# Performance work log

Hardware: AMD Instinct MI355X
Metric: run time of the kernel (lower is better)

Reference implementation:

```python
import jax, jax.numpy as jnp
import numpy as np


def _shift(w):
    # max(0, -min(w)): scalar shift making w + shift non-negative
    return jnp.maximum(0.0, -jnp.min(w))


def shifted_linear(x, W, b=None):
    # F.linear with non-negative weights plus row-sum correction
    alpha = _shift(W)
    y = x @ (W + alpha).T - alpha * jnp.sum(x, axis=-1, keepdims=True)
    if b is not None:
        y = y + b
    return y


def shifted_depthwise_conv(x, w, b):
    # x: (B, D, L), w: (D, 1, K) depthwise; causal-style padding K-1, sliced to L by caller
    alpha = _shift(w)
    k = w.shape[2]
    pad = k - 1
    dn = ('NCH', 'OIH', 'NCH')
    groups = w.shape[0]
    y = jax.lax.conv_general_dilated(x, w + alpha, (1,), [(pad, pad)],
                                     dimension_numbers=dn, feature_group_count=groups)
    ones_k = jnp.ones_like(w)
    ssum = jax.lax.conv_general_dilated(x, ones_k, (1,), [(pad, pad)],
                                        dimension_numbers=dn, feature_group_count=groups)
    return y - alpha * ssum + b[None, :, None]


def setup_inputs() -> dict:
    key = jax.random.key(0)
    ks = jax.random.split(key, 10)
    d_model, d_inner, d_state, d_conv, dt_rank = 1024, 2048, 16, 4, 64
    B, L = 2, 1024
    s = 0.05
    return {
        'hidden_states': jax.random.normal(ks[0], (B, L, d_model), jnp.float32),
        'W_in': jax.random.normal(ks[1], (2 * d_inner, d_model), jnp.float32) * s,
        'conv_w': jax.random.normal(ks[2], (d_inner, 1, d_conv), jnp.float32) * 0.3,
        'conv_b': jax.random.normal(ks[3], (d_inner,), jnp.float32) * s,
        'W_x': jax.random.normal(ks[4], (dt_rank + 2 * d_state, d_inner), jnp.float32) * s,
        'W_dt': jax.random.normal(ks[5], (d_inner, dt_rank), jnp.float32) * s,
        'dt_bias': jax.random.normal(ks[6], (d_inner,), jnp.float32),
        'W_out': jax.random.normal(ks[7], (d_model, d_inner), jnp.float32) * s,
        'A_log': jax.random.normal(ks[8], (d_inner, d_state), jnp.float32) * 0.5,
        'D': jax.random.normal(ks[9], (d_inner,), jnp.float32),
    }


def reference(hidden_states, W_in, conv_w, conv_b, W_x, W_dt, dt_bias, W_out, A_log, D):
    b, l, dm = hidden_states.shape
    d_inner = conv_w.shape[0]
    d_state = A_log.shape[1]
    dt_rank = W_dt.shape[1]

    A = jnp.exp(A_log)  # (d_inner, d_state), always positive

    # in_proj over (b*l, d_model) -> (b, 2*d_inner, l)
    xz = shifted_linear(hidden_states.reshape(b * l, dm), W_in)
    xz = xz.reshape(b, l, 2 * d_inner).transpose(0, 2, 1)
    x, z = xz[:, :d_inner], xz[:, d_inner:]

    # depthwise shifted conv + SiLU activation, truncated to seqlen
    x = jax.nn.silu(shifted_depthwise_conv(x, conv_w, conv_b)[..., :l])

    # x_proj -> dt_raw, B, C
    x_dbl = shifted_linear(x.transpose(0, 2, 1).reshape(b * l, d_inner), W_x)
    dt_raw = x_dbl[:, :dt_rank]
    Bm = x_dbl[:, dt_rank:dt_rank + d_state].reshape(b, l, d_state).transpose(0, 2, 1)  # (b,n,l)
    Cm = x_dbl[:, dt_rank + d_state:].reshape(b, l, d_state).transpose(0, 2, 1)         # (b,n,l)
    dt = shifted_linear(dt_raw, W_dt).reshape(b, l, d_inner).transpose(0, 2, 1)          # (b,d,l)

    # delta activation (softplus) with bias, clamped
    delta = jnp.clip(jax.nn.softplus(dt + dt_bias[None, :, None]), 1e-4, 20.0)

    # global scalar shifts for B and C
    beta = _shift(Bm)
    gamma = _shift(Cm)
    B_nn = Bm + beta
    C_nn = Cm + gamma

    # precomputed per-step operands, scan axis first: (l, b, d, n)
    deltaA = jnp.exp(-jnp.einsum('bdl,dn->lbdn', delta, A))
    dBu = jnp.einsum('bdl,bnl,bdl->lbdn', delta, B_nn, x)
    C_scan = C_nn.transpose(2, 0, 1)  # (l, b, n)

    def step(xc, inp):
        dA_i, dBu_i, C_i = inp
        xc = dA_i * xc + dBu_i                                   # (b,d,n)
        y = jnp.einsum('bdn,bn->bd', xc, C_i) - gamma * jnp.sum(xc, axis=-1)
        return xc, y

    x0 = jnp.zeros((b, d_inner, d_state), dtype=delta.dtype)
    _, ys = jax.lax.scan(step, x0, (deltaA, dBu, C_scan))        # ys: (l, b, d)

    y = ys.transpose(1, 2, 0) + x * D[None, :, None]             # (b, d, l) skip term
    y = y * jax.nn.silu(z)                                       # gate activation

    out = shifted_linear(y.transpose(0, 2, 1).reshape(b * l, d_inner), W_out)
    return out.reshape(b, l, dm)
```

## Files before the change

kernel.cpp:

```cpp
#include <hip/hip_runtime.h>
#include <hip/hip_bf16.h>
#include <math.h>

#define DM 1024
#define DI 2048
#define DS 16
#define DTR 64
#define NB 2
#define LL 1024
#define TT (NB*LL)
#define SCH 16
#define NCH (LL/SCH)

typedef unsigned short u16;
typedef __attribute__((ext_vector_type(8))) short bf16x8;
typedef __attribute__((ext_vector_type(4))) float f32x4;

#define LOG2E 1.4426950408889634f

__device__ inline u16 f2bf(float f) {
  union { float f; unsigned u; } c; c.f = f;
  unsigned u = c.u;
  return (u16)((u + 0x7fffu + ((u >> 16) & 1u)) >> 16);
}

#define GLDS16(g, l) __builtin_amdgcn_global_load_lds( \
    (const __attribute__((address_space(1))) unsigned int*)(g), \
    (__attribute__((address_space(3))) unsigned int*)(l), 16, 0, 0)

template<int BM, int BN>
__global__ __launch_bounds__(256) void gemm_bf16(
    const u16* __restrict__ A, const u16* __restrict__ B,
    float* __restrict__ C, int M, int N, int K) {
  constexpr int WAVES_M = BM / 64;
  constexpr int WAVES_N = 4 / WAVES_M;
  constexpr int WTM = 4;
  constexpr int WTN = BN / (WAVES_N * 16);
  constexpr int ASLABS = BM / 16;
  constexpr int SLABS = (BM + BN) / 16;
  constexpr int SPW = SLABS / 4;
  __shared__ u16 As[BM * 32];
  __shared__ u16 Bs[BN * 32];
  const int tid = threadIdx.x;
  const int wave = tid >> 6;
  const int lane = tid & 63;
  const int bm = blockIdx.y * BM;
  const int bn = blockIdx.x * BN;
  const int wm = (wave / WAVES_N) * 64;
  const int wn = (wave % WAVES_N) * (WTN * 16);
  const int r4 = lane >> 2;
  const int kc = (lane & 3) * 8;
  const int fr = lane & 15;
  const int fq = lane >> 4;

  f32x4 acc[WTM][WTN];
#pragma unroll
  for (int i = 0; i < WTM; ++i)
#pragma unroll
    for (int j = 0; j < WTN; ++j) acc[i][j] = (f32x4){0.f, 0.f, 0.f, 0.f};

  for (int k0 = 0; k0 < K; k0 += 32) {
#pragma unroll
    for (int s = wave * SPW; s < (wave + 1) * SPW; ++s) {
      if (s < ASLABS) {
        int row = s * 16 + r4;
        GLDS16(A + (size_t)(bm + row) * K + k0 + kc, &As[s * 512]);
      } else {
        int row = (s - ASLABS) * 16 + r4;
        GLDS16(B + (size_t)(bn + row) * K + k0 + kc, &Bs[(s - ASLABS) * 512]);
      }
    }
    __syncthreads();
    bf16x8 af[WTM], bf[WTN];
#pragma unroll
    for (int i = 0; i < WTM; ++i)
      af[i] = *(const bf16x8*)&As[(wm + 16 * i + fr) * 32 + fq * 8];
#pragma unroll
    for (int j = 0; j < WTN; ++j)
      bf[j] = *(const bf16x8*)&Bs[(wn + 16 * j + fr) * 32 + fq * 8];
#pragma unroll
    for (int i = 0; i < WTM; ++i)
#pragma unroll
      for (int j = 0; j < WTN; ++j)
        acc[i][j] = __builtin_amdgcn_mfma_f32_16x16x32_bf16(af[i], bf[j], acc[i][j], 0, 0, 0);
    __syncthreads();
  }

#pragma unroll
  for (int i = 0; i < WTM; ++i) {
    int row0 = bm + wm + 16 * i + fq * 4;
#pragma unroll
    for (int j = 0; j < WTN; ++j) {
      int col = bn + wn + 16 * j + fr;
#pragma unroll
      for (int r = 0; r < 4; ++r)
        C[(size_t)(row0 + r) * N + col] = acc[i][j][r];
    }
  }
}

template<int EPI>
__global__ __launch_bounds__(256) void gemm_bt(
    const float* __restrict__ A, const float* __restrict__ B,
    float* __restrict__ C, int M, int N,
    int lda, int ldb, int ldc, const float* __restrict__ bias, int kz) {
  __shared__ float As[16][65];
  __shared__ float Bs[16][65];
  const int tid = threadIdx.x;
  const int bm = blockIdx.y * 64;
  const int bn = blockIdx.x * 64;
  const int ty = tid >> 4;
  const int tx = tid & 15;
  const int koff = blockIdx.z * kz;
  C += (size_t)blockIdx.z * M * ldc;
  float acc[4][4] = {{0.f}};

  for (int k0 = koff; k0 < koff + kz; k0 += 16) {
#pragma unroll
    for (int i = 0; i < 4; ++i) {
      int e = tid + 256 * i;
      int r = e >> 4, c = e & 15;
      As[c][r] = A[(size_t)(bm + r) * lda + k0 + c];
    }
#pragma unroll
    for (int i = 0; i < 4; ++i) {
      int e = tid + 256 * i;
      int r = e >> 4, c = e & 15;
      int gn = bn + r;
      Bs[c][r] = (gn < N) ? B[(size_t)gn * ldb + k0 + c] : 0.0f;
    }
    __syncthreads();
#pragma unroll
    for (int k = 0; k < 16; ++k) {
      float a[4], bb[4];
#pragma unroll
      for (int i = 0; i < 4; ++i) a[i] = As[k][ty + 16 * i];
#pragma unroll
      for (int j = 0; j < 4; ++j) bb[j] = Bs[k][tx + 16 * j];
#pragma unroll
      for (int i = 0; i < 4; ++i)
#pragma unroll
        for (int j = 0; j < 4; ++j) acc[i][j] += a[i] * bb[j];
    }
    __syncthreads();
  }

#pragma unroll
  for (int i = 0; i < 4; ++i) {
    int m = bm + ty + 16 * i;
#pragma unroll
    for (int j = 0; j < 4; ++j) {
      int n = bn + tx + 16 * j;
      if (n < N) {
        float v = acc[i][j];
        if (EPI == 1) {
          v += bias[n];
          float sp = (v > 20.0f) ? v : log1pf(expf(v));
          v = fminf(fmaxf(sp, 1e-4f), 20.0f);
        }
        C[(size_t)m * ldc + n] = v;
      }
    }
  }
}

__global__ __launch_bounds__(256) void gemm3_reduce(
    const float* __restrict__ part, float* __restrict__ xdb) {
  int i = blockIdx.x * 256 + threadIdx.x;
  float s = 0.f;
#pragma unroll
  for (int z = 0; z < 8; ++z) s += part[(size_t)z * TT * 96 + i];
  xdb[i] = s;
}

__global__ __launch_bounds__(256) void cast_all(
    const float* __restrict__ hs, const float* __restrict__ win,
    const float* __restrict__ wout, u16* __restrict__ hs_bf,
    u16* __restrict__ win_bf, u16* __restrict__ wout_bf) {
  int gid = blockIdx.x * 256 + threadIdx.x;
  const float* src; u16* dst; int off;
  if (gid < 524288)        { src = hs;   dst = hs_bf;   off = gid; }
  else if (gid < 1572864)  { src = win;  dst = win_bf;  off = gid - 524288; }
  else                     { src = wout; dst = wout_bf; off = gid - 1572864; }
  float4 v = ((const float4*)src)[off];
  ushort4 o;
  o.x = f2bf(v.x); o.y = f2bf(v.y); o.z = f2bf(v.z); o.w = f2bf(v.w);
  ((ushort4*)dst)[off] = o;
}

__global__ __launch_bounds__(256) void conv_silu4(
    const float* __restrict__ xz, const float* __restrict__ w,
    const float* __restrict__ cb, float* __restrict__ xc) {
  int gid = blockIdx.x * 256 + threadIdx.x;
  int dq = (gid & 511) * 4;
  int t = gid >> 9;
  int l = t & (LL - 1);
  float wv[4][4];
#pragma unroll
  for (int j = 0; j < 4; ++j) {
    float4 ww = *(const float4*)&w[(dq + j) * 4];
    wv[j][0] = ww.x; wv[j][1] = ww.y; wv[j][2] = ww.z; wv[j][3] = ww.w;
  }
  float4 acc = *(const float4*)&cb[dq];
#pragma unroll
  for (int k = 0; k < 4; ++k) {
    int ll = l - 3 + k;
    if (ll < 0) continue;
    float4 xv = *(const float4*)&xz[(size_t)(t - 3 + k) * (2 * DI) + dq];
    acc.x += xv.x * wv[0][k]; acc.y += xv.y * wv[1][k];
    acc.z += xv.z * wv[2][k]; acc.w += xv.w * wv[3][k];
  }
  acc.x /= (1.0f + expf(-acc.x)); acc.y /= (1.0f + expf(-acc.y));
  acc.z /= (1.0f + expf(-acc.z)); acc.w /= (1.0f + expf(-acc.w));
  *(float4*)&xc[(size_t)t * DI + dq] = acc;
}

__global__ __launch_bounds__(256) void beta_part(
    const float* __restrict__ xdb, float* __restrict__ pmin) {
  float mn = 3.4e38f;
  for (int i = blockIdx.x * 256 + threadIdx.x; i < TT * DS; i += 64 * 256) {
    int t = i >> 4, n = i & 15;
    mn = fminf(mn, xdb[t * 96 + 64 + n]);
  }
#pragma unroll
  for (int o = 32; o; o >>= 1) mn = fminf(mn, __shfl_down(mn, o));
  __shared__ float sm[4];
  if ((threadIdx.x & 63) == 0) sm[threadIdx.x >> 6] = mn;
  __syncthreads();
  if (threadIdx.x == 0)
    pmin[blockIdx.x] = fminf(fminf(sm[0], sm[1]), fminf(sm[2], sm[3]));
}

__global__ void beta_fin(const float* __restrict__ pmin, float* __restrict__ beta) {
  float mn = pmin[threadIdx.x];
#pragma unroll
  for (int o = 32; o; o >>= 1) mn = fminf(mn, __shfl_down(mn, o));
  if (threadIdx.x == 0) beta[0] = fmaxf(0.0f, -mn);
}

__global__ __launch_bounds__(256) void scan_pass1(
    const float* __restrict__ delta, const float* __restrict__ xc,
    const float* __restrict__ xdb, const float* __restrict__ A_log,
    const float* __restrict__ beta_p,
    float* __restrict__ hend, float* __restrict__ Ssum) {
  const int d = blockIdx.x * 256 + threadIdx.x;
  const int c = blockIdx.y;
  const int b = blockIdx.z;
  __shared__ float Bsh[SCH][16];
  const float beta = beta_p[0];
  const int t0 = b * LL + c * SCH;
  {
    int i = threadIdx.x;
    int tt = i >> 4, n = i & 15;
    Bsh[tt][n] = xdb[(size_t)(t0 + tt) * 96 + 64 + n] + beta;
  }
  __syncthreads();
  float Av2[16];
#pragma unroll
  for (int n = 0; n < 16; ++n) Av2[n] = expf(A_log[d * 16 + n]) * LOG2E;
  float h[16];
#pragma unroll
  for (int n = 0; n < 16; ++n) h[n] = 0.f;
  float S = 0.f;
  for (int tt = 0; tt < SCH; ++tt) {
    int t = t0 + tt;
    float dv = delta[(size_t)t * DI + d];
    float xv = xc[(size_t)t * DI + d];
    float dx = dv * xv;
    S += dv;
#pragma unroll
    for (int n = 0; n < 16; ++n) {
      float a = __builtin_amdgcn_exp2f(-dv * Av2[n]);
      h[n] = a * h[n] + dx * Bsh[tt][n];
    }
  }
  size_t base = (((size_t)(b * NCH + c) * DI) + d) * 16;
#pragma unroll
  for (int n = 0; n < 16; ++n) hend[base + n] = h[n];
  Ssum[((size_t)(b * NCH + c) * DI) + d] = S;
}

__global__ __launch_bounds__(256) void scan_pass2(
    float* __restrict__ hend, const float* __restrict__ Ssum,
    const float* __restrict__ A_log) {
  int gid = blockIdx.x * 256 + threadIdx.x;
  int n = gid & 15;
  int d = (gid >> 4) & (DI - 1);
  int b = gid >> 15;
  float Av2 = expf(A_log[d * 16 + n]) * LOG2E;
  float H = 0.f;
  for (int c = 0; c < NCH; ++c) {
    size_t cb = ((size_t)(b * NCH + c) * DI) + d;
    float hl = hend[cb * 16 + n];
    float p = __builtin_amdgcn_exp2f(-Av2 * Ssum[cb]);
    hend[cb * 16 + n] = H;
    H = p * H + hl;
  }
}

__global__ __launch_bounds__(256) void scan_pass3(
    const float* __restrict__ delta, const float* __restrict__ xc,
    const float* __restrict__ xdb, const float* __restrict__ xz,
    const float* __restrict__ A_log, const float* __restrict__ Dp,
    const float* __restrict__ beta_p, const float* __restrict__ hstart,
    u16* __restrict__ ybf) {
  const int d = blockIdx.x * 256 + threadIdx.x;
  const int c = blockIdx.y;
  const int b = blockIdx.z;
  __shared__ float Bsh[SCH][16];
  __shared__ float Csh[SCH][16];
  const float beta = beta_p[0];
  const int t0 = b * LL + c * SCH;
  {
    int i = threadIdx.x;
    int tt = i >> 4, n = i & 15;
    size_t row = (size_t)(t0 + tt) * 96;
    Bsh[tt][n] = xdb[row + 64 + n] + beta;
    Csh[tt][n] = xdb[row + 80 + n];
  }
  __syncthreads();
  float Av2[16];
#pragma unroll
  for (int n = 0; n < 16; ++n) Av2[n] = expf(A_log[d * 16 + n]) * LOG2E;
  float h[16];
  size_t base = (((size_t)(b * NCH + c) * DI) + d) * 16;
#pragma unroll
  for (int n = 0; n < 16; ++n) h[n] = hstart[base + n];
  const float Dd = Dp[d];
  for (int tt = 0; tt < SCH; ++tt) {
    int t = t0 + tt;
    float dv = delta[(size_t)t * DI + d];
    float xv = xc[(size_t)t * DI + d];
    float dx = dv * xv;
    float yv = 0.f;
#pragma unroll
    for (int n = 0; n < 16; ++n) {
      float a = __builtin_amdgcn_exp2f(-dv * Av2[n]);
      h[n] = a * h[n] + dx * Bsh[tt][n];
      yv += h[n] * Csh[tt][n];
    }
    float zv = xz[(size_t)t * (2 * DI) + DI + d];
    float out = (yv + xv * Dd) * (zv / (1.0f + expf(-zv)));
    ybf[(size_t)t * DI + d] = f2bf(out);
  }
}

extern "C" void kernel_launch(void* const* d_in, const int* in_sizes, int n_in,
                              void* d_out, int out_size, void* d_ws, size_t ws_size,
                              hipStream_t stream) {
  const float* hs      = (const float*)d_in[0];
  const float* W_in    = (const float*)d_in[1];
  const float* conv_w  = (const float*)d_in[2];
  const float* conv_b  = (const float*)d_in[3];
  const float* W_x     = (const float*)d_in[4];
  const float* W_dt    = (const float*)d_in[5];
  const float* dt_bias = (const float*)d_in[6];
  const float* W_out   = (const float*)d_in[7];
  const float* A_log   = (const float*)d_in[8];
  const float* Dp      = (const float*)d_in[9];
  float* out = (float*)d_out;

  float* ws     = (float*)d_ws;
  float* xz     = ws;
  float* xcv    = xz   + (size_t)TT * 2 * DI;
  float* xdb    = xcv  + (size_t)TT * DI;
  float* dlt    = xdb  + (size_t)TT * 96;
  float* betab  = dlt  + (size_t)TT * DI;
  float* pmin   = betab + 64;
  float* hend   = pmin + 64;
  float* Ssum   = hend + (size_t)NB * NCH * DI * 16;
  float* hs_bfR = Ssum + (size_t)NB * NCH * DI;
  float* win_bfR  = hs_bfR + (size_t)TT * DM / 2;
  float* wout_bfR = win_bfR + (size_t)2 * DI * DM / 2;

  u16* hs_bf   = (u16*)hs_bfR;
  u16* win_bf  = (u16*)win_bfR;
  u16* wout_bf = (u16*)wout_bfR;
  u16* ybf     = (u16*)win_bfR;
  float* part  = dlt;

  dim3 blk(256);

  cast_all<<<8192, blk, 0, stream>>>(hs, W_in, W_out, hs_bf, win_bf, wout_bf);

  gemm_bf16<128, 128><<<dim3(4096 / 128, TT / 128), blk, 0, stream>>>(
      hs_bf, win_bf, xz, TT, 2 * DI, DM);

  conv_silu4<<<(TT * DI / 4) / 256, blk, 0, stream>>>(xz, conv_w, conv_b, xcv);

  gemm_bt<0><<<dim3(2, TT / 64, 8), blk, 0, stream>>>(
      xcv, W_x, part, TT, 96, DI, DI, 96, nullptr, 256);
  gemm3_reduce<<<(TT * 96) / 256, blk, 0, stream>>>(part, xdb);

  beta_part<<<64, blk, 0, stream>>>(xdb, pmin);
  beta_fin<<<1, 64, 0, stream>>>(pmin, betab);

  gemm_bt<1><<<dim3(DI / 64, TT / 64), blk, 0, stream>>>(
      xdb, W_dt, dlt, TT, DI, 96, DTR, DI, dt_bias, DTR);

  scan_pass1<<<dim3(DI / 256, NCH, NB), blk, 0, stream>>>(
      dlt, xcv, xdb, A_log, betab, hend, Ssum);
  scan_pass2<<<(NB * DI * DS) / 256, blk, 0, stream>>>(hend, Ssum, A_log);
  scan_pass3<<<dim3(DI / 256, NCH, NB), blk, 0, stream>>>(
      dlt, xcv, xdb, xz, A_log, Dp, betab, hend, ybf);

  gemm_bf16<64, 128><<<dim3(DM / 128, TT / 64), blk, 0, stream>>>(
      ybf, wout_bf, out, TT, DM, DI);
}
```

Measured before the change: 293.3 us.

## Move x_proj and dt_proj GEMMs onto bf16 MFMA kernel with split-K

Replaces the fp32 SIMT gemm_bt kernels for the x_proj and dt_proj projections with the bf16 MFMA gemm_bf16 kernel. It also adds a split-K (blockIdx.z) path and a fused softplus epilogue. The conv kernel now also writes a bf16 copy of its activations. The cast kernel converts W_x (zero-padded to 128 rows) and W_dt to bf16, and the reduce kernel emits bf16 dt inputs. This targets the slow scalar fp32 GEMMs at the cost of extra bf16 stores, 16-way partial sums, and reduced precision in delta and B/C.

After: 277.9 us. 5.3% less time.

```diff
diff --git a/kernel.cpp b/kernel.cpp
--- a/kernel.cpp
+++ b/kernel.cpp
@@ -28,10 +28,11 @@
     (const __attribute__((address_space(1))) unsigned int*)(g), \
     (__attribute__((address_space(3))) unsigned int*)(l), 16, 0, 0)
 
-template<int BM, int BN>
+template<int BM, int BN, int EPI>
 __global__ __launch_bounds__(256) void gemm_bf16(
     const u16* __restrict__ A, const u16* __restrict__ B,
-    float* __restrict__ C, int M, int N, int K) {
+    float* __restrict__ C, int M, int N, int K, int kpb,
+    const float* __restrict__ bias) {
   constexpr int WAVES_M = BM / 64;
   constexpr int WAVES_N = 4 / WAVES_M;
   constexpr int WTM = 4;
@@ -52,6 +53,8 @@
   const int kc = (lane & 3) * 8;
   const int fr = lane & 15;
   const int fq = lane >> 4;
+  const int koff = blockIdx.z * kpb;
+  C += (size_t)blockIdx.z * M * N;
 
   f32x4 acc[WTM][WTN];
 #pragma unroll
@@ -59,7 +62,7 @@
 #pragma unroll
     for (int j = 0; j < WTN; ++j) acc[i][j] = (f32x4){0.f, 0.f, 0.f, 0.f};
 
-  for (int k0 = 0; k0 < K; k0 += 32) {
+  for (int k0 = koff; k0 < koff + kpb; k0 += 32) {
 #pragma unroll
     for (int s = wave * SPW; s < (wave + 1) * SPW; ++s) {
       if (s < ASLABS) {
@@ -93,95 +96,50 @@
     for (int j = 0; j < WTN; ++j) {
       int col = bn + wn + 16 * j + fr;
 #pragma unroll
-      for (int r = 0; r < 4; ++r)
-        C[(size_t)(row0 + r) * N + col] = acc[i][j][r];
-    }
-  }
-}
-
-template<int EPI>
-__global__ __launch_bounds__(256) void gemm_bt(
-    const float* __restrict__ A, const float* __restrict__ B,
-    float* __restrict__ C, int M, int N,
-    int lda, int ldb, int ldc, const float* __restrict__ bias, int kz) {
-  __shared__ float As[16][65];
-  __shared__ float Bs[16][65];
-  const int tid = threadIdx.x;
-  const int bm = blockIdx.y * 64;
-  const int bn = blockIdx.x * 64;
-  const int ty = tid >> 4;
-  const int tx = tid & 15;
-  const int koff = blockIdx.z * kz;
-  C += (size_t)blockIdx.z * M * ldc;
-  float acc[4][4] = {{0.f}};
-
-  for (int k0 = koff; k0 < koff + kz; k0 += 16) {
-#pragma unroll
-    for (int i = 0; i < 4; ++i) {
-      int e = tid + 256 * i;
-      int r = e >> 4, c = e & 15;
-      As[c][r] = A[(size_t)(bm + r) * lda + k0 + c];
-    }
-#pragma unroll
-    for (int i = 0; i < 4; ++i) {
-      int e = tid + 256 * i;
-      int r = e >> 4, c = e & 15;
-      int gn = bn + r;
-      Bs[c][r] = (gn < N) ? B[(size_t)gn * ldb + k0 + c] : 0.0f;
-    }
-    __syncthreads();
-#pragma unroll
-    for (int k = 0; k < 16; ++k) {
-      float a[4], bb[4];
-#pragma unroll
-      for (int i = 0; i < 4; ++i) a[i] = As[k][ty + 16 * i];
-#pragma unroll
-      for (int j = 0; j < 4; ++j) bb[j] = Bs[k][tx + 16 * j];
-#pragma unroll
-      for (int i = 0; i < 4; ++i)
-#pragma unroll
-        for (int j = 0; j < 4; ++j) acc[i][j] += a[i] * bb[j];
-    }
-    __syncthreads();
-  }
-
-#pragma unroll
-  for (int i = 0; i < 4; ++i) {
-    int m = bm + ty + 16 * i;
-#pragma unroll
-    for (int j = 0; j < 4; ++j) {
-      int n = bn + tx + 16 * j;
-      if (n < N) {
-        float v = acc[i][j];
+      for (int r = 0; r < 4; ++r) {
+        float v = acc[i][j][r];
         if (EPI == 1) {
-          v += bias[n];
+          v += bias[col];
           float sp = (v > 20.0f) ? v : log1pf(expf(v));
           v = fminf(fmaxf(sp, 1e-4f), 20.0f);
         }
-        C[(size_t)m * ldc + n] = v;
+        C[(size_t)(row0 + r) * N + col] = v;
       }
     }
   }
 }
 
 __global__ __launch_bounds__(256) void gemm3_reduce(
-    const float* __restrict__ part, float* __restrict__ xdb) {
+    const float* __restrict__ part, float* __restrict__ xdb,
+    u16* __restrict__ dtraw_bf) {
   int i = blockIdx.x * 256 + threadIdx.x;
+  int t = i >> 7, col = i & 127;
   float s = 0.f;
 #pragma unroll
-  for (int z = 0; z < 8; ++z) s += part[(size_t)z * TT * 96 + i];
-  xdb[i] = s;
+  for (int z = 0; z < 16; ++z) s += part[(size_t)z * TT * 128 + i];
+  if (col < 96) xdb[t * 96 + col] = s;
+  if (col < 64) dtraw_bf[t * 64 + col] = f2bf(s);
 }
 
 __global__ __launch_bounds__(256) void cast_all(
     const float* __restrict__ hs, const float* __restrict__ win,
-    const float* __restrict__ wout, u16* __restrict__ hs_bf,
-    u16* __restrict__ win_bf, u16* __restrict__ wout_bf) {
+    const float* __restrict__ wout, const float* __restrict__ wx,
+    const float* __restrict__ wdt,
+    u16* __restrict__ hs_bf, u16* __restrict__ win_bf,
+    u16* __restrict__ wout_bf, u16* __restrict__ wx_bf,
+    u16* __restrict__ wdt_bf) {
   int gid = blockIdx.x * 256 + threadIdx.x;
   const float* src; u16* dst; int off;
-  if (gid < 524288)        { src = hs;   dst = hs_bf;   off = gid; }
-  else if (gid < 1572864)  { src = win;  dst = win_bf;  off = gid - 524288; }
-  else                     { src = wout; dst = wout_bf; off = gid - 1572864; }
+  if (gid < 524288)       { src = hs;   dst = hs_bf;   off = gid; }
+  else if (gid < 1572864) { src = win;  dst = win_bf;  off = gid - 524288; }
+  else if (gid < 2097152) { src = wout; dst = wout_bf; off = gid - 1572864; }
+  else if (gid < 2146304) { src = wx;   dst = wx_bf;   off = gid - 2097152; }
+  else if (gid < 2179072) { src = wdt;  dst = wdt_bf;  off = gid - 2146304; }
+  else {
+    ushort4 z4 = {0, 0, 0, 0};
+    ((ushort4*)wx_bf)[49152 + gid - 2179072] = z4;
+    return;
+  }
   float4 v = ((const float4*)src)[off];
   ushort4 o;
   o.x = f2bf(v.x); o.y = f2bf(v.y); o.z = f2bf(v.z); o.w = f2bf(v.w);
@@ -190,7 +148,8 @@
 
 __global__ __launch_bounds__(256) void conv_silu4(
     const float* __restrict__ xz, const float* __restrict__ w,
-    const float* __restrict__ cb, float* __restrict__ xc) {
+    const float* __restrict__ cb, float* __restrict__ xc,
+    u16* __restrict__ xc_bf) {
   int gid = blockIdx.x * 256 + threadIdx.x;
   int dq = (gid & 511) * 4;
   int t = gid >> 9;
@@ -213,6 +172,9 @@
   acc.x /= (1.0f + expf(-acc.x)); acc.y /= (1.0f + expf(-acc.y));
   acc.z /= (1.0f + expf(-acc.z)); acc.w /= (1.0f + expf(-acc.w));
   *(float4*)&xc[(size_t)t * DI + dq] = acc;
+  ushort4 o;
+  o.x = f2bf(acc.x); o.y = f2bf(acc.y); o.z = f2bf(acc.z); o.w = f2bf(acc.w);
+  *(ushort4*)&xc_bf[(size_t)t * DI + dq] = o;
 }
 
 __global__ __launch_bounds__(256) void beta_part(
@@ -372,31 +334,40 @@
   float* hs_bfR = Ssum + (size_t)NB * NCH * DI;
   float* win_bfR  = hs_bfR + (size_t)TT * DM / 2;
   float* wout_bfR = win_bfR + (size_t)2 * DI * DM / 2;
-
-  u16* hs_bf   = (u16*)hs_bfR;
-  u16* win_bf  = (u16*)win_bfR;
-  u16* wout_bf = (u16*)wout_bfR;
-  u16* ybf     = (u16*)win_bfR;
-  float* part  = dlt;
+  float* xcv_bfR  = wout_bfR + (size_t)DM * DI / 2;
+  float* wx_bfR   = xcv_bfR + (size_t)TT * DI / 2;
+  float* wdt_bfR  = wx_bfR + 131072;
+  float* dtraw_bfR = wdt_bfR + 65536;
+
+  u16* hs_bf    = (u16*)hs_bfR;
+  u16* win_bf   = (u16*)win_bfR;
+  u16* wout_bf  = (u16*)wout_bfR;
+  u16* xcv_bf   = (u16*)xcv_bfR;
+  u16* wx_bf    = (u16*)wx_bfR;
+  u16* wdt_bf   = (u16*)wdt_bfR;
+  u16* dtraw_bf = (u16*)dtraw_bfR;
+  u16* ybf      = (u16*)win_bfR;
+  float* part   = dlt;
 
   dim3 blk(256);
 
-  cast_all<<<8192, blk, 0, stream>>>(hs, W_in, W_out, hs_bf, win_bf, wout_bf);
-
-  gemm_bf16<128, 128><<<dim3(4096 / 128, TT / 128), blk, 0, stream>>>(
-      hs_bf, win_bf, xz, TT, 2 * DI, DM);
-
-  conv_silu4<<<(TT * DI / 4) / 256, blk, 0, stream>>>(xz, conv_w, conv_b, xcv);
-
-  gemm_bt<0><<<dim3(2, TT / 64, 8), blk, 0, stream>>>(
-      xcv, W_x, part, TT, 96, DI, DI, 96, nullptr, 256);
-  gemm3_reduce<<<(TT * 96) / 256, blk, 0, stream>>>(part, xdb);
+  cast_all<<<8576, blk, 0, stream>>>(hs, W_in, W_out, W_x, W_dt,
+                                     hs_bf, win_bf, wout_bf, wx_bf, wdt_bf);
+
+  gemm_bf16<128, 128, 0><<<dim3(4096 / 128, TT / 128), blk, 0, stream>>>(
+      hs_bf, win_bf, xz, TT, 2 * DI, DM, DM, nullptr);
+
+  conv_silu4<<<(TT * DI / 4) / 256, blk, 0, stream>>>(xz, conv_w, conv_b, xcv, xcv_bf);
+
+  gemm_bf16<128, 128, 0><<<dim3(1, TT / 128, 16), blk, 0, stream>>>(
+      xcv_bf, wx_bf, part, TT, 128, DI, 128, nullptr);
+  gemm3_reduce<<<(TT * 128) / 256, blk, 0, stream>>>(part, xdb, dtraw_bf);
 
   beta_part<<<64, blk, 0, stream>>>(xdb, pmin);
   beta_fin<<<1, 64, 0, stream>>>(pmin, betab);
 
-  gemm_bt<1><<<dim3(DI / 64, TT / 64), blk, 0, stream>>>(
-      xdb, W_dt, dlt, TT, DI, 96, DTR, DI, dt_bias, DTR);
+  gemm_bf16<128, 128, 1><<<dim3(DI / 128, TT / 128), blk, 0, stream>>>(
+      dtraw_bf, wdt_bf, dlt, TT, DI, DTR, DTR, dt_bias);
 
   scan_pass1<<<dim3(DI / 256, NCH, NB), blk, 0, stream>>>(
       dlt, xcv, xdb, A_log, betab, hend, Ssum);
@@ -404,6 +375,6 @@
   scan_pass3<<<dim3(DI / 256, NCH, NB), blk, 0, stream>>>(
       dlt, xcv, xdb, xz, A_log, Dp, betab, hend, ybf);
 
-  gemm_bf16<64, 128><<<dim3(DM / 128, TT / 64), blk, 0, stream>>>(
-      ybf, wout_bf, out, TT, DM, DI);
-}
+  gemm_bf16<64, 128, 0><<<dim3(DM / 128, TT / 64), blk, 0, stream>>>(
+      ybf, wout_bf, out, TT, DM, DI, DI, nullptr);
+}
```
